# Optimization experiments

Hardware: AMD Instinct MI355X
Metric: run time of the kernel (lower is better)

## Reference

```python
import math
import jax, jax.numpy as jnp
import numpy as np

B, S, H, NH, BS, R = 2, 4096, 1024, 16, 64, 3
HD = H // NH          # 64 head dim
L = S // BS           # 64 blocks
PEN = -10000.0


def _make_rand_attn():
    # data-independent random block plan (like HF bigbird, seeded numpy),
    # per head, per middle query block: R random key blocks excluding
    # global blocks (0, L-1) and the sliding window (i-1, i, i+1)
    rng = np.random.RandomState(42)
    ra = np.zeros((NH, L - 2, R), dtype=np.int64)
    for h in range(NH):
        for i in range(1, L - 1):
            choices = np.array([j for j in range(L) if j not in (0, i - 1, i, i + 1, L - 1)])
            ra[h, i - 1] = rng.choice(choices, R, replace=False)
    return ra


def setup_inputs():
    key = jax.random.key(0)
    ks = jax.random.split(key, 8)
    sc = 1.0 / math.sqrt(H)
    return {
        "Q": jax.random.normal(ks[0], (B, S, H), jnp.float32),
        "K": jax.random.normal(ks[1], (B, S, H), jnp.float32),
        "V": jax.random.normal(ks[2], (B, S, H), jnp.float32),
        "mask": jnp.ones((B, S), jnp.float32),
        "Wq": jax.random.normal(ks[3], (H, H), jnp.float32) * sc,
        "bq": jnp.zeros((H,), jnp.float32),
        "Wk": jax.random.normal(ks[4], (H, H), jnp.float32) * sc,
        "bk": jnp.zeros((H,), jnp.float32),
        "Wv": jax.random.normal(ks[5], (H, H), jnp.float32) * sc,
        "bv": jnp.zeros((H,), jnp.float32),
        "rand_attn": jnp.asarray(_make_rand_attn()),
    }


def _forward(Q, K, V, mask, Wq, bq, Wk, bk, Wv, bv, rand_attn):
    rsd = 1.0 / math.sqrt(HD)
    sm = lambda x: jax.nn.softmax(x, axis=-1)

    def proj(x, W, b):  # torch Linear: x @ W^T + b, then split heads
        return (x @ W.T + b).reshape(B, S, NH, HD).transpose(0, 2, 1, 3)

    q = proj(Q, Wq, bq)  # [B,NH,S,HD]
    k = proj(K, Wk, bk)
    v = proj(V, Wv, bv)
    qb = q.reshape(B, NH, L, BS, HD)
    kb = k.reshape(B, NH, L, BS, HD)
    vb = v.reshape(B, NH, L, BS, HD)

    # ---- masks (derived from padding mask, as in HF create_masks_...) ----
    blocked = mask.reshape(B, L, BS)
    from_mask = mask[:, None, :, None]   # [B,1,S,1]
    to_mask = mask[:, None, None, :]     # [B,1,1,S]
    exp_to = jnp.concatenate([blocked[:, 1:-3], blocked[:, 2:-2], blocked[:, 3:-1]], axis=2)  # [B,L-4,3BS]
    band_mask = jnp.einsum('blq,blk->blqk', blocked[:, 2:-2], exp_to)[:, None]  # [B,1,L-4,BS,3BS]

    ra = jnp.broadcast_to(rand_attn[None], (B, NH, L - 2, R))
    bidx = jnp.arange(B)[:, None, None, None]
    hidx = jnp.arange(NH)[None, :, None, None]
    gk = kb[bidx, hidx, ra].reshape(B, NH, L - 2, R * BS, HD)  # gathered random key blocks
    gv = vb[bidx, hidx, ra].reshape(B, NH, L - 2, R * BS, HD)
    rm = blocked[bidx, ra].reshape(B, NH, L - 2, R * BS)
    rand_mask = jnp.einsum('blq,bhlk->bhlqk', blocked[:, 1:-1], rm)  # [B,NH,L-2,BS,R*BS]

    # ---- first block: dense attention over all keys ----
    p1 = jnp.einsum('bhqd,bhkd->bhqk', qb[:, :, 0], k) * rsd + (1.0 - to_mask) * PEN
    ctx_first = jnp.einsum('bhqk,bhkd->bhqd', sm(p1), v)

    # ---- second block: global(0) + window(1,2) + last + random ----
    k2 = jnp.concatenate([kb[:, :, 0], kb[:, :, 1], kb[:, :, 2], kb[:, :, -1], gk[:, :, 0]], axis=2)
    v2 = jnp.concatenate([vb[:, :, 0], vb[:, :, 1], vb[:, :, 2], vb[:, :, -1], gv[:, :, 0]], axis=2)
    p2 = jnp.einsum('bhqd,bhkd->bhqk', qb[:, :, 1], k2) * rsd
    seq_pad2 = jnp.concatenate([to_mask[..., :3 * BS], to_mask[..., -BS:],
                                jnp.ones((B, 1, 1, R * BS), mask.dtype)], axis=3)
    rand_pad2 = jnp.concatenate([jnp.ones((B, NH, BS, 4 * BS), mask.dtype), rand_mask[:, :, 0]], axis=3)
    p2 = p2 + (1.0 - jnp.minimum(seq_pad2, rand_pad2)) * PEN
    ctx_second = jnp.einsum('bhqk,bhkd->bhqd', sm(p2), v2)

    # ---- middle blocks: band (3 sliding) + random + 2 global ----
    exp_k = jnp.concatenate([kb[:, :, 1:-3], kb[:, :, 2:-2], kb[:, :, 3:-1]], axis=3)  # [B,NH,L-4,3BS,HD]
    exp_v = jnp.concatenate([vb[:, :, 1:-3], vb[:, :, 2:-2], vb[:, :, 3:-1]], axis=3)
    mq = qb[:, :, 2:-2]
    inner = jnp.einsum('bhlqd,bhlkd->bhlqk', mq, exp_k) * rsd + (1.0 - band_mask) * PEN
    randp = jnp.einsum('bhlqd,bhlkd->bhlqk', mq, gk[:, :, 1:-1]) * rsd + (1.0 - rand_mask[:, :, 1:-1]) * PEN
    firstp = jnp.einsum('bhlqd,bhkd->bhlqk', mq, kb[:, :, 0]) * rsd + (1.0 - to_mask[:, :, :, None, :BS]) * PEN
    lastp = jnp.einsum('bhlqd,bhkd->bhlqk', mq, kb[:, :, -1]) * rsd + (1.0 - to_mask[:, :, :, None, -BS:]) * PEN
    w = sm(jnp.concatenate([firstp, inner, randp, lastp], axis=-1))  # [B,NH,L-4,BS,(5+R)*BS]
    ctx_mid = jnp.einsum('bhlqk,bhlkd->bhlqd', w[..., BS:4 * BS], exp_v)
    ctx_mid += jnp.einsum('bhlqk,bhlkd->bhlqd', w[..., 4 * BS:(4 + R) * BS], gv[:, :, 1:-1])
    ctx_mid += jnp.einsum('bhlqk,bhkd->bhlqd', w[..., :BS], vb[:, :, 0])
    ctx_mid += jnp.einsum('bhlqk,bhkd->bhlqd', w[..., -BS:], vb[:, :, -1])

    # ---- second-to-last block ----
    k3 = jnp.concatenate([kb[:, :, 0], kb[:, :, -3], kb[:, :, -2], kb[:, :, -1], gk[:, :, -1]], axis=2)
    v3 = jnp.concatenate([vb[:, :, 0], vb[:, :, -3], vb[:, :, -2], vb[:, :, -1], gv[:, :, -1]], axis=2)
    p3 = jnp.einsum('bhqd,bhkd->bhqk', qb[:, :, -2], k3) * rsd
    seq_pad3 = jnp.concatenate([to_mask[..., :BS], to_mask[..., -3 * BS:],
                                jnp.ones((B, 1, 1, R * BS), mask.dtype)], axis=3)
    rand_pad3 = jnp.concatenate([jnp.ones((B, NH, BS, 4 * BS), mask.dtype), rand_mask[:, :, -1]], axis=3)
    p3 = p3 + (1.0 - jnp.minimum(seq_pad3, rand_pad3)) * PEN
    ctx_seclast = jnp.einsum('bhqk,bhkd->bhqd', sm(p3), v3)

    # ---- last block: dense attention over all keys ----
    p4 = jnp.einsum('bhqd,bhkd->bhqk', qb[:, :, -1], k) * rsd + (1.0 - to_mask) * PEN
    ctx_last = jnp.einsum('bhqk,bhkd->bhqd', sm(p4), v)

    ctx = jnp.concatenate([ctx_first[:, :, None], ctx_second[:, :, None], ctx_mid,
                           ctx_seclast[:, :, None], ctx_last[:, :, None]], axis=2)
    ctx = ctx.reshape(B, NH, S, HD) * from_mask
    return ctx.transpose(0, 2, 1, 3).reshape(B, S, NH * HD)


def reference(Q, K, V, mask, Wq, bq, Wk, bk, Wv, bv, rand_attn):
    return _forward(Q, K, V, mask, Wq, bq, Wk, bk, Wv, bv, rand_attn)
```

## Files before the change

### kernel.cpp

```cpp
#include <hip/hip_runtime.h>
#include <hip/hip_bf16.h>
#include <stdint.h>

#define BB 2
#define SS 4096
#define HH 1024
#define NHh 16
#define HD 64
#define LL 64
#define BS 64
#define RR 3
#define PENf (-10000.0f)

typedef unsigned int uint;
typedef __attribute__((ext_vector_type(8))) short bf16x8;
typedef __attribute__((ext_vector_type(4))) float f32x4;

__device__ __forceinline__ ushort f2bf(float f) {
    union { float f; uint u; } v; v.f = f;
    uint u = v.u;
    return (ushort)((u + 0x7fffu + ((u >> 16) & 1u)) >> 16);
}
__device__ __forceinline__ uint pack_bf(float a, float b) {
    return (uint)f2bf(a) | (((uint)f2bf(b)) << 16);
}
__device__ __forceinline__ uint scale_pair(uint w) {
    float lo = __uint_as_float(w << 16) * 0.125f;
    float hi = __uint_as_float(w & 0xffff0000u) * 0.125f;
    return (uint)f2bf(lo) | (((uint)f2bf(hi)) << 16);
}
__device__ __forceinline__ uint4 scale4(uint4 w) {
    uint4 o;
    o.x = scale_pair(w.x); o.y = scale_pair(w.y);
    o.z = scale_pair(w.z); o.w = scale_pair(w.w);
    return o;
}
__device__ __forceinline__ void async16(const ushort* g, ushort* l) {
    __builtin_amdgcn_global_load_lds((const __attribute__((address_space(1))) uint*)g,
                                     (__attribute__((address_space(3))) uint*)l,
                                     16, 0, 0);
}

__global__ __launch_bounds__(256)
void cvt_kernel(const float* __restrict__ Xq, const float* __restrict__ Xk,
                const float* __restrict__ Xv, const float* __restrict__ Wq,
                const float* __restrict__ Wk, const float* __restrict__ Wv,
                ushort* __restrict__ Xbf, ushort* __restrict__ Wbf)
{
    const size_t XTOT = (size_t)3 * BB * SS * HH;
    const uint u = blockIdx.x * 256 + threadIdx.x;
    const size_t e = (size_t)u * 8;
    const float* src; ushort* dst;
    if (e < XTOT) {
        const int zz = (int)(e >> 23);
        src = (zz == 0 ? Xq : zz == 1 ? Xk : Xv) + (e & ((1u << 23) - 1));
        dst = Xbf + e;
    } else {
        const size_t e2 = e - XTOT;
        const int zz = (int)(e2 >> 20);
        src = (zz == 0 ? Wq : zz == 1 ? Wk : Wv) + (e2 & ((1u << 20) - 1));
        dst = Wbf + e2;
    }
    float4 a = ((const float4*)src)[0];
    float4 c = ((const float4*)src)[1];
    uint4 o;
    o.x = pack_bf(a.x, a.y); o.y = pack_bf(a.z, a.w);
    o.z = pack_bf(c.x, c.y); o.w = pack_bf(c.z, c.w);
    *(uint4*)dst = o;
}

__global__ __launch_bounds__(256)
void gemm3_kernel(const ushort* __restrict__ Xbf, const ushort* __restrict__ Wbf,
                  const float* __restrict__ bq, const float* __restrict__ bk,
                  const float* __restrict__ bv,
                  ushort* __restrict__ qb, ushort* __restrict__ kb,
                  ushort* __restrict__ vbT)
{
    __shared__ __align__(16) ushort smem[128 * 136];
    ushort* As = smem;
    ushort* Bs = smem + 8192;

    const int z = blockIdx.z;
    const ushort* A  = Xbf + (size_t)z * ((size_t)BB * SS * HH);
    const ushort* Bt = Wbf + (size_t)z * (HH * HH);
    const float* bias = (z == 0) ? bq : (z == 1) ? bk : bv;

    const int tid = threadIdx.x;
    const int m0 = blockIdx.x * 128;
    const int n0 = blockIdx.y * 128;
    const int wave = tid >> 6;
    const int lane = tid & 63;
    const int l15 = lane & 15;
    const int quad = lane >> 4;
    const int wr = wave >> 1, wc = wave & 1;

    f32x4 acc[4][4];
#pragma unroll
    for (int i = 0; i < 4; ++i)
#pragma unroll
        for (int j = 0; j < 4; ++j) acc[i][j] = (f32x4){0.f, 0.f, 0.f, 0.f};

    const int p8 = (lane & 3) * 8;
    const ushort* Abase = A + (size_t)(m0 + wave * 32 + (lane >> 2)) * HH + p8;
    const ushort* Bbase = Bt + (size_t)(n0 + wave * 32 + (lane >> 2)) * HH + p8;

#define STAGE_G(k0, bp)                                        \
    do {                                                       \
        ushort* A0 = As + (bp) * 4096 + wave * 1024;           \
        ushort* B0 = Bs + (bp) * 4096 + wave * 1024;           \
        async16(Abase + (k0), A0);                             \
        async16(Abase + 16 * HH + (k0), A0 + 512);             \
        async16(Bbase + (k0), B0);                             \
        async16(Bbase + 16 * HH + (k0), B0 + 512);             \
    } while (0)

    STAGE_G(0, 0);
    for (int k0 = 0, bp = 0; k0 < HH; k0 += 32, bp ^= 1) {
        __syncthreads();
        if (k0 + 32 < HH) STAGE_G(k0 + 32, bp ^ 1);
        bf16x8 af[4], bfr[4];
#pragma unroll
        for (int mt = 0; mt < 4; ++mt)
            af[mt] = *(const bf16x8*)(As + bp * 4096 + (wr * 64 + mt * 16 + l15) * 32 + quad * 8);
#pragma unroll
        for (int nt = 0; nt < 4; ++nt)
            bfr[nt] = *(const bf16x8*)(Bs + bp * 4096 + (wc * 64 + nt * 16 + l15) * 32 + quad * 8);
        if (z < 2) {
#pragma unroll
            for (int i = 0; i < 4; ++i)
#pragma unroll
                for (int j = 0; j < 4; ++j)
                    acc[i][j] = __builtin_amdgcn_mfma_f32_16x16x32_bf16(bfr[i], af[j], acc[i][j], 0, 0, 0);
        } else {
#pragma unroll
            for (int i = 0; i < 4; ++i)
#pragma unroll
                for (int j = 0; j < 4; ++j)
                    acc[i][j] = __builtin_amdgcn_mfma_f32_16x16x32_bf16(af[i], bfr[j], acc[i][j], 0, 0, 0);
        }
    }
#undef STAGE_G

    if (z < 2) {
        ushort* outp = (z == 0) ? qb : kb;
#pragma unroll
        for (int wt = 0; wt < 4; ++wt) {
            const int n_base = n0 + wc * 64 + wt * 16 + quad * 4;
            const float4 b4 = *(const float4*)&bias[n_base];
            const int nh = n_base >> 6;
            const int hd = n_base & 63;
#pragma unroll
            for (int xt = 0; xt < 4; ++xt) {
                const int m = m0 + wr * 64 + xt * 16 + l15;
                const int bgl = m >> 12, s = m & 4095;
                uint2 pk;
                pk.x = pack_bf(acc[wt][xt][0] + b4.x, acc[wt][xt][1] + b4.y);
                pk.y = pack_bf(acc[wt][xt][2] + b4.z, acc[wt][xt][3] + b4.w);
                *(uint2*)&outp[((size_t)((bgl << 4) | nh) * SS + s) * HD + hd] = pk;
            }
        }
    } else {
        __syncthreads();
        ushort* stg = smem;
#pragma unroll
        for (int nt = 0; nt < 4; ++nt) {
            const int n_local = wc * 64 + nt * 16 + l15;
            const float bn = bias[n0 + n_local];
#pragma unroll
            for (int mt = 0; mt < 4; ++mt) {
                const int m_base = wr * 64 + mt * 16 + quad * 4;
                uint2 pk;
                pk.x = pack_bf(acc[mt][nt][0] + bn, acc[mt][nt][1] + bn);
                pk.y = pack_bf(acc[mt][nt][2] + bn, acc[mt][nt][3] + bn);
                *(uint2*)(stg + n_local * 136 + m_base) = pk;
            }
        }
        __syncthreads();
        const int n_row = tid >> 1;
        const int half = tid & 1;
        const int n = n0 + n_row;
        const int nh = n >> 6, hd = n & 63;
        const int bgl = m0 >> 12;
        const int sbase = (m0 & 4095) + half * 64;
        const uint4* src = (const uint4*)(stg + n_row * 136 + half * 64);
        uint4* dst = (uint4*)(vbT + ((size_t)((bgl << 4) | nh) * HD + hd) * SS + sbase);
#pragma unroll
        for (int j = 0; j < 8; ++j) dst[j] = src[j];
    }
}

__global__ __launch_bounds__(256)
void proj3_kernel(const float* __restrict__ Xq, const float* __restrict__ Xk,
                  const float* __restrict__ Xv,
                  const float* __restrict__ Wq, const float* __restrict__ Wk,
                  const float* __restrict__ Wv,
                  const float* __restrict__ bq, const float* __restrict__ bk,
                  const float* __restrict__ bv,
                  ushort* __restrict__ qb, ushort* __restrict__ kb,
                  ushort* __restrict__ vbT)
{
    __shared__ __align__(16) ushort smem[128 * 136];
    ushort* As = smem;
    ushort* Bs = smem + 128 * 40;

    const int z = blockIdx.z;
    const float* X    = (z == 0) ? Xq : (z == 1) ? Xk : Xv;
    const float* W    = (z == 0) ? Wq : (z == 1) ? Wk : Wv;
    const float* bias = (z == 0) ? bq : (z == 1) ? bk : bv;

    const int tid = threadIdx.x;
    const int m0 = blockIdx.x * 128;
    const int n0 = blockIdx.y * 128;
    const int wave = tid >> 6;
    const int lane = tid & 63;
    const int l15 = lane & 15;
    const int quad = lane >> 4;
    const int wr = wave >> 1, wc = wave & 1;

    f32x4 acc[4][4];
#pragma unroll
    for (int mt = 0; mt < 4; ++mt)
#pragma unroll
        for (int nt = 0; nt < 4; ++nt) acc[mt][nt] = (f32x4){0.f, 0.f, 0.f, 0.f};

    const int srow = tid >> 1;
    const int shalf = tid & 1;
    const float* xp = X + (size_t)(m0 + srow) * HH + shalf * 16;
    const float* wp = W + (size_t)(n0 + srow) * HH + shalf * 16;
    ushort* asw = As + srow * 40 + shalf * 16;
    ushort* bsw = Bs + srow * 40 + shalf * 16;

    for (int k0 = 0; k0 < HH; k0 += 32) {
        float4 a0 = *(const float4*)(xp + k0);
        float4 a1 = *(const float4*)(xp + k0 + 4);
        float4 a2 = *(const float4*)(xp + k0 + 8);
        float4 a3 = *(const float4*)(xp + k0 + 12);
        float4 b0 = *(const float4*)(wp + k0);
        float4 b1 = *(const float4*)(wp + k0 + 4);
        float4 b2 = *(const float4*)(wp + k0 + 8);
        float4 b3 = *(const float4*)(wp + k0 + 12);
        __syncthreads();
        uint4 pa, pb;
        pa.x = pack_bf(a0.x, a0.y); pa.y = pack_bf(a0.z, a0.w);
        pa.z = pack_bf(a1.x, a1.y); pa.w = pack_bf(a1.z, a1.w);
        *(uint4*)asw = pa;
        pa.x = pack_bf(a2.x, a2.y); pa.y = pack_bf(a2.z, a2.w);
        pa.z = pack_bf(a3.x, a3.y); pa.w = pack_bf(a3.z, a3.w);
        *(uint4*)(asw + 8) = pa;
        pb.x = pack_bf(b0.x, b0.y); pb.y = pack_bf(b0.z, b0.w);
        pb.z = pack_bf(b1.x, b1.y); pb.w = pack_bf(b1.z, b1.w);
        *(uint4*)bsw = pb;
        pb.x = pack_bf(b2.x, b2.y); pb.y = pack_bf(b2.z, b2.w);
        pb.z = pack_bf(b3.x, b3.y); pb.w = pack_bf(b3.z, b3.w);
        *(uint4*)(bsw + 8) = pb;
        __syncthreads();

        bf16x8 af[4], bfr[4];
#pragma unroll
        for (int mt = 0; mt < 4; ++mt)
            af[mt] = *(const bf16x8*)(As + (wr * 64 + mt * 16 + l15) * 40 + quad * 8);
#pragma unroll
        for (int nt = 0; nt < 4; ++nt)
            bfr[nt] = *(const bf16x8*)(Bs + (wc * 64 + nt * 16 + l15) * 40 + quad * 8);
#pragma unroll
        for (int mt = 0; mt < 4; ++mt)
#pragma unroll
            for (int nt = 0; nt < 4; ++nt)
                acc[mt][nt] = __builtin_amdgcn_mfma_f32_16x16x32_bf16(af[mt], bfr[nt], acc[mt][nt], 0, 0, 0);
    }

    if (z < 2) {
        ushort* outp = (z == 0) ? qb : kb;
#pragma unroll
        for (int nt = 0; nt < 4; ++nt) {
            const int n = n0 + wc * 64 + nt * 16 + l15;
            const float bn = bias[n];
            const int nh = n >> 6, hd = n & 63;
#pragma unroll
            for (int mt = 0; mt < 4; ++mt) {
#pragma unroll
                for (int rr = 0; rr < 4; ++rr) {
                    const int m = m0 + wr * 64 + mt * 16 + quad * 4 + rr;
                    const int bgl = m >> 12, s = m & 4095;
                    outp[((size_t)((bgl << 4) | nh) * SS + s) * HD + hd] = f2bf(acc[mt][nt][rr] + bn);
                }
            }
        }
    } else {
        __syncthreads();
        ushort* stg = smem;
#pragma unroll
        for (int nt = 0; nt < 4; ++nt) {
            const int n_local = wc * 64 + nt * 16 + l15;
            const float bn = bias[n0 + n_local];
#pragma unroll
            for (int mt = 0; mt < 4; ++mt) {
                const int m_base = wr * 64 + mt * 16 + quad * 4;
                uint2 pk;
                pk.x = pack_bf(acc[mt][nt][0] + bn, acc[mt][nt][1] + bn);
                pk.y = pack_bf(acc[mt][nt][2] + bn, acc[mt][nt][3] + bn);
                *(uint2*)(stg + n_local * 136 + m_base) = pk;
            }
        }
        __syncthreads();
        const int n_row = tid >> 1;
        const int half = tid & 1;
        const int n = n0 + n_row;
        const int nh = n >> 6, hd = n & 63;
        const int bgl = m0 >> 12;
        const int sbase = (m0 & 4095) + half * 64;
        const uint4* src = (const uint4*)(stg + n_row * 136 + half * 64);
        uint4* dst = (uint4*)(vbT + ((size_t)((bgl << 4) | nh) * HD + hd) * SS + sbase);
#pragma unroll
        for (int j = 0; j < 8; ++j) dst[j] = src[j];
    }
}

__global__ __launch_bounds__(256)
void attn_kernel(const ushort* __restrict__ qg, const ushort* __restrict__ kg,
                 const ushort* __restrict__ vTg,
                 const float* __restrict__ mask, const int* __restrict__ rand_attn,
                 float* __restrict__ out, float* __restrict__ partO,
                 float* __restrict__ partML)
{
    __shared__ __align__(16) ushort qs_ps[64][72];
    __shared__ __align__(16) ushort ks2[2][2][64][32];
    __shared__ __align__(16) ushort vs2[2][2][64][32];
    __shared__ __align__(16) float qm_s[64];
    __shared__ __align__(16) float km_s[2][64];

    const int tid = threadIdx.x;
    const int wid = blockIdx.x;
    const int bh = wid / 78;
    const int r = wid - bh * 78;
    const int b = bh >> 4, h = bh & 15;

    int i, nkb;
    int kbl[8], pfl[8];
    bool dense;
    int part = 0, which = 0;
    if (r < 62) {
        dense = false;
        i = r + 1;
        const int* ra = rand_attn + ((size_t)h * (LL - 2) + (i - 1)) * RR;
        if (i == 1) {
            kbl[0] = 0; kbl[1] = 1; kbl[2] = 2; kbl[3] = LL - 1;
            kbl[4] = ra[0]; kbl[5] = ra[1]; kbl[6] = ra[2]; kbl[7] = 0;
            pfl[0] = pfl[1] = pfl[2] = pfl[3] = 0;
            pfl[4] = pfl[5] = pfl[6] = 1; pfl[7] = 0;
            nkb = 7;
        } else if (i == LL - 2) {
            kbl[0] = 0; kbl[1] = LL - 3; kbl[2] = LL - 2; kbl[3] = LL - 1;
            kbl[4] = ra[0]; kbl[5] = ra[1]; kbl[6] = ra[2]; kbl[7] = 0;
            pfl[0] = pfl[1] = pfl[2] = pfl[3] = 0;
            pfl[4] = pfl[5] = pfl[6] = 1; pfl[7] = 0;
            nkb = 7;
        } else {
            kbl[0] = 0;      pfl[0] = 0;
            kbl[1] = i - 1;  pfl[1] = 1;
            kbl[2] = i;      pfl[2] = 1;
            kbl[3] = i + 1;  pfl[3] = 1;
            kbl[4] = LL - 1; pfl[4] = 0;
            kbl[5] = ra[0]; kbl[6] = ra[1]; kbl[7] = ra[2];
            pfl[5] = pfl[6] = pfl[7] = 1;
            nkb = 8;
        }
    } else {
        dense = true;
        const int r2 = r - 62;
        which = r2 >> 3;
        part = r2 & 7;
        i = which ? (LL - 1) : 0;
        nkb = 8;
#pragma unroll
        for (int j = 0; j < 8; ++j) { kbl[j] = part * 8 + j; pfl[j] = 0; }
    }

    const int lane = tid & 63;
    const int wave = tid >> 6;
    const int l15 = lane & 15;
    const int quad = lane >> 4;
    const int srow = lane >> 2;
    const int p8 = (lane & 3) * 8;
    const ushort* kgb = kg + (size_t)bh * SS * HD;
    const ushort* vgb = vTg + (size_t)bh * HD * SS;

#define STAGE_KV(kb_, bp)                                                        \
    do {                                                                         \
        const size_t krow = (size_t)((kb_) * BS + wave * 16 + srow) * HD;        \
        async16(kgb + krow + p8,      &ks2[bp][0][wave * 16][0]);                \
        async16(kgb + krow + 32 + p8, &ks2[bp][1][wave * 16][0]);                \
        const size_t vrow = (size_t)(wave * 16 + srow) * SS + (kb_) * BS;        \
        async16(vgb + vrow + p8,      &vs2[bp][0][wave * 16][0]);                \
        async16(vgb + vrow + 32 + p8, &vs2[bp][1][wave * 16][0]);                \
    } while (0)

    {
        const int row = tid >> 2;
        const int c0 = (tid & 3) * 16;
        const ushort* src = qg + ((size_t)bh * SS + i * BS + row) * HD + c0;
        uint4 w0 = *(const uint4*)src;
        uint4 w1 = *(const uint4*)(src + 8);
        *(uint4*)&qs_ps[row][c0] = scale4(w0);
        *(uint4*)&qs_ps[row][c0 + 8] = scale4(w1);
        if (tid < 64) qm_s[tid] = mask[(size_t)b * SS + i * BS + tid];
    }
    STAGE_KV(kbl[0], 0);
    if (tid < 64) km_s[0][tid] = mask[(size_t)b * SS + kbl[0] * BS + tid];
    __syncthreads();

    bf16x8 aq[2];
    aq[0] = *(const bf16x8*)&qs_ps[wave * 16 + l15][quad * 8];
    aq[1] = *(const bf16x8*)&qs_ps[wave * 16 + l15][32 + quad * 8];
    const float qm = qm_s[wave * 16 + l15];

    float mrow = -1e30f, lrow = 0.0f;
    f32x4 accO[4];
#pragma unroll
    for (int dt = 0; dt < 4; ++dt) accO[dt] = (f32x4){0.f, 0.f, 0.f, 0.f};

    for (int it = 0; it < nkb; ++it) {
        const int cur = it & 1;
        if (it + 1 < nkb) {
            STAGE_KV(kbl[it + 1], cur ^ 1);
            if (tid < 64) km_s[cur ^ 1][tid] = mask[(size_t)b * SS + kbl[it + 1] * BS + tid];
        }
        const int pf = pfl[it];

        f32x4 sc[4];
#pragma unroll
        for (int nt = 0; nt < 4; ++nt) sc[nt] = (f32x4){0.f, 0.f, 0.f, 0.f};
#pragma unroll
        for (int c = 0; c < 2; ++c) {
#pragma unroll
            for (int nt = 0; nt < 4; ++nt) {
                bf16x8 af = *(const bf16x8*)&ks2[cur][c][nt * 16 + l15][quad * 8];
                sc[nt] = __builtin_amdgcn_mfma_f32_16x16x32_bf16(af, aq[c], sc[nt], 0, 0, 0);
            }
        }

        float p[4][4];
        float bm = -1e30f;
#pragma unroll
        for (int nt = 0; nt < 4; ++nt) {
            const float4 km4 = *(const float4*)&km_s[cur][nt * 16 + quad * 4];
            const float kmv[4] = {km4.x, km4.y, km4.z, km4.w};
#pragma unroll
            for (int rr = 0; rr < 4; ++rr) {
                const float pm = pf ? (qm * kmv[rr]) : kmv[rr];
                const float sv = sc[nt][rr] + (1.0f - pm) * PENf;
                p[nt][rr] = sv;
                bm = fmaxf(bm, sv);
            }
        }
        bm = fmaxf(bm, __shfl_xor(bm, 16));
        bm = fmaxf(bm, __shfl_xor(bm, 32));
        const float mn = fmaxf(mrow, bm);
        const float alpha = __expf(mrow - mn);
        mrow = mn;
        float ls = 0.0f;
#pragma unroll
        for (int nt = 0; nt < 4; ++nt)
#pragma unroll
            for (int rr = 0; rr < 4; ++rr) {
                p[nt][rr] = __expf(p[nt][rr] - mn);
                ls += p[nt][rr];
            }
        ls += __shfl_xor(ls, 16);
        ls += __shfl_xor(ls, 32);
        lrow = lrow * alpha + ls;

#pragma unroll
        for (int nt = 0; nt < 4; ++nt) {
            uint2 pk;
            pk.x = pack_bf(p[nt][0], p[nt][1]);
            pk.y = pack_bf(p[nt][2], p[nt][3]);
            *(uint2*)&qs_ps[wave * 16 + l15][nt * 16 + quad * 4] = pk;
        }
        float a4[4];
#pragma unroll
        for (int rr = 0; rr < 4; ++rr) a4[rr] = __shfl(alpha, quad * 4 + rr, 64);
#pragma unroll
        for (int dt = 0; dt < 4; ++dt) {
#pragma unroll
            for (int rr = 0; rr < 4; ++rr) accO[dt][rr] *= a4[rr];
        }

#pragma unroll
        for (int c = 0; c < 2; ++c) {
            bf16x8 ap = *(const bf16x8*)&qs_ps[wave * 16 + l15][c * 32 + quad * 8];
#pragma unroll
            for (int dt = 0; dt < 4; ++dt) {
                bf16x8 bvf = *(const bf16x8*)&vs2[cur][c][dt * 16 + l15][quad * 8];
                accO[dt] = __builtin_amdgcn_mfma_f32_16x16x32_bf16(ap, bvf, accO[dt], 0, 0, 0);
            }
        }

        if (it + 1 < nkb) __syncthreads();
    }
#undef STAGE_KV

    if (!dense) {
#pragma unroll
        for (int rr = 0; rr < 4; ++rr) {
            const int qloc = quad * 4 + rr;
            const float lq = __shfl(lrow, qloc, 64);
            const float inv = qm_s[wave * 16 + qloc] / lq;
#pragma unroll
            for (int dt = 0; dt < 4; ++dt) {
                const int d = dt * 16 + l15;
                out[((size_t)b * SS + i * BS + wave * 16 + qloc) * HH + h * HD + d] = accO[dt][rr] * inv;
            }
        }
    } else {
        const int slot = (bh * 2 + which) * 8 + part;
        float* po = partO + (size_t)slot * 4096;
#pragma unroll
        for (int rr = 0; rr < 4; ++rr) {
            const int qrow = wave * 16 + quad * 4 + rr;
#pragma unroll
            for (int dt = 0; dt < 4; ++dt) {
                const int d = dt * 16 + l15;
                po[qrow * 64 + d] = accO[dt][rr];
            }
        }
        if (lane < 16) {
            partML[slot * 128 + wave * 16 + lane] = mrow;
            partML[slot * 128 + 64 + wave * 16 + lane] = lrow;
        }
    }
}

__global__ __launch_bounds__(256)
void combine_kernel(const float* __restrict__ partO, const float* __restrict__ partML,
                    const float* __restrict__ mask, float* __restrict__ out)
{
    const int g = blockIdx.x;
    const int bh = g >> 1, which = g & 1;
    const int b = bh >> 4, h = bh & 15;
    const int i = which ? (LL - 1) : 0;
    const int t = threadIdx.x;
    const int row = t >> 2;
    const int d0 = (t & 3) * 16;
    const int base = g * 8;

    float mp[8], lp[8];
    float M = -1e30f;
#pragma unroll
    for (int p = 0; p < 8; ++p) {
        mp[p] = partML[(base + p) * 128 + row];
        lp[p] = partML[(base + p) * 128 + 64 + row];
        M = fmaxf(M, mp[p]);
    }
    float L = 0.0f, w[8];
#pragma unroll
    for (int p = 0; p < 8; ++p) { w[p] = __expf(mp[p] - M); L += lp[p] * w[p]; }

    float4 o[4];
#pragma unroll
    for (int j = 0; j < 4; ++j) o[j] = make_float4(0.f, 0.f, 0.f, 0.f);
#pragma unroll
    for (int p = 0; p < 8; ++p) {
        const float* po = partO + (size_t)(base + p) * 4096 + row * 64 + d0;
#pragma unroll
        for (int j = 0; j < 4; ++j) {
            float4 v = *(const float4*)(po + j * 4);
            o[j].x = fmaf(w[p], v.x, o[j].x);
            o[j].y = fmaf(w[p], v.y, o[j].y);
            o[j].z = fmaf(w[p], v.z, o[j].z);
            o[j].w = fmaf(w[p], v.w, o[j].w);
        }
    }
    const float fm = mask[(size_t)b * SS + i * BS + row];
    const float inv = fm / L;
    float* dst = out + ((size_t)b * SS + i * BS + row) * HH + h * HD + d0;
#pragma unroll
    for (int j = 0; j < 4; ++j) {
        float4 v;
        v.x = o[j].x * inv; v.y = o[j].y * inv;
        v.z = o[j].z * inv; v.w = o[j].w * inv;
        *(float4*)(dst + j * 4) = v;
    }
}

extern "C" void kernel_launch(void* const* d_in, const int* in_sizes, int n_in,
                              void* d_out, int out_size, void* d_ws, size_t ws_size,
                              hipStream_t stream) {
    (void)in_sizes; (void)n_in; (void)out_size;
    const float* Q    = (const float*)d_in[0];
    const float* K    = (const float*)d_in[1];
    const float* V    = (const float*)d_in[2];
    const float* mask = (const float*)d_in[3];
    const float* Wq   = (const float*)d_in[4];
    const float* bq   = (const float*)d_in[5];
    const float* Wk   = (const float*)d_in[6];
    const float* bk   = (const float*)d_in[7];
    const float* Wv   = (const float*)d_in[8];
    const float* bv   = (const float*)d_in[9];
    const int*   ra   = (const int*)d_in[10];
    float* out = (float*)d_out;

    const size_t qkv = (size_t)BB * NHh * SS * HD;
    ushort* qb  = (ushort*)d_ws;
    ushort* kb  = qb + qkv;
    ushort* vbT = kb + qkv;
    float* partO  = (float*)(vbT + qkv);
    float* partML = partO + (size_t)512 * 4096;
    ushort* Xbf = (ushort*)(partML + (size_t)512 * 128);
    ushort* Wbf = Xbf + 3 * qkv;
    const size_t need = (size_t)((char*)(Wbf + (size_t)3 * HH * HH) - (char*)d_ws);

    if (ws_size >= need) {
        cvt_kernel<<<13824, 256, 0, stream>>>(Q, K, V, Wq, Wk, Wv, Xbf, Wbf);
        gemm3_kernel<<<dim3(64, 8, 3), 256, 0, stream>>>(Xbf, Wbf, bq, bk, bv, qb, kb, vbT);
    } else {
        proj3_kernel<<<dim3(64, 8, 3), 256, 0, stream>>>(Q, K, V, Wq, Wk, Wv, bq, bk, bv,
                                                         qb, kb, vbT);
    }
    attn_kernel<<<dim3(BB * NHh * 78), 256, 0, stream>>>(qb, kb, vbT, mask, ra,
                                                         out, partO, partML);
    combine_kernel<<<dim3(BB * NHh * 2), 256, 0, stream>>>(partO, partML, mask, out);
}
```

Measured before the change: 302.1 us.

## Swizzle K/V LDS, lazy softmax rescale, hardware bf16 pack, split combine blocks

Applies an XOR swizzle to the K/V LDS staging and MFMA operand reads to cut bank conflicts. Skips the online-softmax rescale of the accumulator unless a wave's running max rises by more than 8, avoiding exp and shuffle work on most iterations. Replaces the software bf16 rounding with the v_cvt_pk_bf16_f32 instruction and splits the combine kernel into four times as many 64-thread blocks. The lazy rescale lets exponents grow up to e^8 before renormalising, which changes rounding slightly.

```diff
diff --git a/kernel.cpp b/kernel.cpp
--- a/kernel.cpp
+++ b/kernel.cpp
@@ -22,12 +22,14 @@
     return (ushort)((u + 0x7fffu + ((u >> 16) & 1u)) >> 16);
 }
 __device__ __forceinline__ uint pack_bf(float a, float b) {
-    return (uint)f2bf(a) | (((uint)f2bf(b)) << 16);
+    uint r;
+    asm("v_cvt_pk_bf16_f32 %0, %1, %2" : "=v"(r) : "v"(a), "v"(b));
+    return r;
 }
 __device__ __forceinline__ uint scale_pair(uint w) {
     float lo = __uint_as_float(w << 16) * 0.125f;
     float hi = __uint_as_float(w & 0xffff0000u) * 0.125f;
-    return (uint)f2bf(lo) | (((uint)f2bf(hi)) << 16);
+    return pack_bf(lo, hi);
 }
 __device__ __forceinline__ uint4 scale4(uint4 w) {
     uint4 o;
@@ -381,18 +383,18 @@
     const int l15 = lane & 15;
     const int quad = lane >> 4;
     const int srow = lane >> 2;
-    const int p8 = (lane & 3) * 8;
+    const int p8s = (((lane & 3) ^ ((srow >> 1) & 3))) * 8;
     const ushort* kgb = kg + (size_t)bh * SS * HD;
     const ushort* vgb = vTg + (size_t)bh * HD * SS;
 
 #define STAGE_KV(kb_, bp)                                                        \
     do {                                                                         \
         const size_t krow = (size_t)((kb_) * BS + wave * 16 + srow) * HD;        \
-        async16(kgb + krow + p8,      &ks2[bp][0][wave * 16][0]);                \
-        async16(kgb + krow + 32 + p8, &ks2[bp][1][wave * 16][0]);                \
+        async16(kgb + krow + p8s,      &ks2[bp][0][wave * 16][0]);               \
+        async16(kgb + krow + 32 + p8s, &ks2[bp][1][wave * 16][0]);               \
         const size_t vrow = (size_t)(wave * 16 + srow) * SS + (kb_) * BS;        \
-        async16(vgb + vrow + p8,      &vs2[bp][0][wave * 16][0]);                \
-        async16(vgb + vrow + 32 + p8, &vs2[bp][1][wave * 16][0]);                \
+        async16(vgb + vrow + p8s,      &vs2[bp][0][wave * 16][0]);               \
+        async16(vgb + vrow + 32 + p8s, &vs2[bp][1][wave * 16][0]);               \
     } while (0)
 
     {
@@ -414,6 +416,8 @@
     aq[1] = *(const bf16x8*)&qs_ps[wave * 16 + l15][32 + quad * 8];
     const float qm = qm_s[wave * 16 + l15];
 
+    const int sqz = (quad ^ ((l15 >> 1) & 3)) * 8;
+
     float mrow = -1e30f, lrow = 0.0f;
     f32x4 accO[4];
 #pragma unroll
@@ -434,7 +438,7 @@
         for (int c = 0; c < 2; ++c) {
 #pragma unroll
             for (int nt = 0; nt < 4; ++nt) {
-                bf16x8 af = *(const bf16x8*)&ks2[cur][c][nt * 16 + l15][quad * 8];
+                bf16x8 af = *(const bf16x8*)&ks2[cur][c][nt * 16 + l15][sqz];
                 sc[nt] = __builtin_amdgcn_mfma_f32_16x16x32_bf16(af, aq[c], sc[nt], 0, 0, 0);
             }
         }
@@ -455,20 +459,31 @@
         }
         bm = fmaxf(bm, __shfl_xor(bm, 16));
         bm = fmaxf(bm, __shfl_xor(bm, 32));
-        const float mn = fmaxf(mrow, bm);
-        const float alpha = __expf(mrow - mn);
-        mrow = mn;
+        if (!__all(bm - mrow <= 8.0f)) {
+            const float mn = fmaxf(mrow, bm);
+            const float alpha = __expf(mrow - mn);
+            mrow = mn;
+            float a4[4];
+#pragma unroll
+            for (int rr = 0; rr < 4; ++rr) a4[rr] = __shfl(alpha, quad * 4 + rr, 64);
+#pragma unroll
+            for (int dt = 0; dt < 4; ++dt) {
+#pragma unroll
+                for (int rr = 0; rr < 4; ++rr) accO[dt][rr] *= a4[rr];
+            }
+            lrow *= alpha;
+        }
         float ls = 0.0f;
 #pragma unroll
         for (int nt = 0; nt < 4; ++nt)
 #pragma unroll
             for (int rr = 0; rr < 4; ++rr) {
-                p[nt][rr] = __expf(p[nt][rr] - mn);
+                p[nt][rr] = __expf(p[nt][rr] - mrow);
                 ls += p[nt][rr];
             }
         ls += __shfl_xor(ls, 16);
         ls += __shfl_xor(ls, 32);
-        lrow = lrow * alpha + ls;
+        lrow += ls;
 
 #pragma unroll
         for (int nt = 0; nt < 4; ++nt) {
@@ -477,21 +492,13 @@
             pk.y = pack_bf(p[nt][2], p[nt][3]);
             *(uint2*)&qs_ps[wave * 16 + l15][nt * 16 + quad * 4] = pk;
         }
-        float a4[4];
-#pragma unroll
-        for (int rr = 0; rr < 4; ++rr) a4[rr] = __shfl(alpha, quad * 4 + rr, 64);
-#pragma unroll
-        for (int dt = 0; dt < 4; ++dt) {
-#pragma unroll
-            for (int rr = 0; rr < 4; ++rr) accO[dt][rr] *= a4[rr];
-        }
 
 #pragma unroll
         for (int c = 0; c < 2; ++c) {
             bf16x8 ap = *(const bf16x8*)&qs_ps[wave * 16 + l15][c * 32 + quad * 8];
 #pragma unroll
             for (int dt = 0; dt < 4; ++dt) {
-                bf16x8 bvf = *(const bf16x8*)&vs2[cur][c][dt * 16 + l15][quad * 8];
+                bf16x8 bvf = *(const bf16x8*)&vs2[cur][c][dt * 16 + l15][sqz];
                 accO[dt] = __builtin_amdgcn_mfma_f32_16x16x32_bf16(ap, bvf, accO[dt], 0, 0, 0);
             }
         }
@@ -531,16 +538,17 @@
     }
 }
 
-__global__ __launch_bounds__(256)
+__global__ __launch_bounds__(64)
 void combine_kernel(const float* __restrict__ partO, const float* __restrict__ partML,
                     const float* __restrict__ mask, float* __restrict__ out)
 {
-    const int g = blockIdx.x;
+    const int g4 = blockIdx.x;
+    const int g = g4 >> 2;
     const int bh = g >> 1, which = g & 1;
     const int b = bh >> 4, h = bh & 15;
     const int i = which ? (LL - 1) : 0;
     const int t = threadIdx.x;
-    const int row = t >> 2;
+    const int row = ((g4 & 3) << 4) | (t >> 2);
     const int d0 = (t & 3) * 16;
     const int base = g * 8;
 
@@ -619,5 +627,5 @@
     }
     attn_kernel<<<dim3(BB * NHh * 78), 256, 0, stream>>>(qb, kb, vbT, mask, ra,
                                                          out, partO, partML);
-    combine_kernel<<<dim3(BB * NHh * 2), 256, 0, stream>>>(partO, partML, mask, out);
-}
+    combine_kernel<<<dim3(BB * NHh * 2 * 4), 64, 0, stream>>>(partO, partML, mask, out);
+}
```

New measurement: 292.3 us. -3.3%, faster.
